# Performance work log

Measured on AMD Instinct MI355X. Metric: run time of the kernel, lower is better.

Reference implementation:

```python
import jax, jax.numpy as jnp
import numpy as np

K = 4096
N = 11008
GROUP_SIZE = 128
NUM_GROUPS = K // GROUP_SIZE
BATCH = 4
SEQ = 2048


def setup_inputs() -> dict:
    key = jax.random.key(0)
    kx, kw, ks = jax.random.split(key, 3)
    x = jax.random.normal(kx, (BATCH, SEQ, K), dtype=jnp.float16)
    # packed uint8 bytes, each holding two INT4 values (stored as int32)
    weight_packed = jax.random.randint(kw, (N, K // 2), 0, 256, dtype=jnp.int32)
    # positive group-wise scales ~ abs(randn)*0.1 -> uniform*0.1 is fine statistically
    scales = (jax.random.uniform(ks, (N, NUM_GROUPS), dtype=jnp.float32) * 0.1).astype(jnp.float16)
    return {"x": x, "weight_packed": weight_packed, "scales": scales}


def _dequantize(weight_packed, scales):
    # unpack: low nibble first, then high nibble -> (N, K) values in [0, 15]
    low = weight_packed & 15
    high = (weight_packed >> 4) & 15
    w_int = jnp.stack([low, high], axis=-1).reshape(weight_packed.shape[0], -1)  # (N, K)
    # symmetric dequant with implicit zero-point 8, group-wise scales
    scales_expanded = jnp.repeat(scales, GROUP_SIZE, axis=1)  # (N, K)
    return scales_expanded * (w_int.astype(jnp.float16) - jnp.float16(8.0))


def reference(x, weight_packed, scales):
    # Y = X @ W_dequant.T : (B, S, K) x (N, K) -> (B, S, N)
    w_dequant = _dequantize(weight_packed, scales)  # (N, K) fp16
    out = jnp.einsum('bsk,nk->bsn', x, w_dequant)
    return out.astype(jnp.float16)
```

## Files before the change

### kernel.cpp

```cpp
#include <hip/hip_runtime.h>
#include <stdint.h>


namespace {

typedef unsigned int u32;
typedef unsigned short u16;
typedef __attribute__((ext_vector_type(8))) short bf16x8;
typedef __attribute__((ext_vector_type(4))) float f32x4;
typedef __attribute__((ext_vector_type(4))) u32 u32x4;

constexpr int Mt = 8192;
constexpr int Nt = 11008;
constexpr int Kt = 4096;
constexpr int KP = Kt / 2;
constexpr int NG = 32;
constexpr int BM = 256;
constexpr int BN = 256;
constexpr int BK = 64;
constexpr int THREADS = 512;
constexpr int GRID = (Mt / BM) * (Nt / BN);
constexpr int NKT = Kt / BK;
constexpr int NB_CNT = Nt / BN;
constexpr int TILE_BYTES = BM * BK * 2;

__device__ __forceinline__ u16 f2bf(float f) {
  u32 u = __float_as_uint(f);
  return (u16)((u + 0x7FFFu + ((u >> 16) & 1u)) >> 16);
}
__device__ __forceinline__ u32 pk2bf(float a, float b) {
  return (u32)f2bf(a) | ((u32)f2bf(b) << 16);
}
__device__ __forceinline__ u32 dqpair(u32 b, float s, float c) {
  float f0 = (float)(b & 15u);
  float f1 = (float)((b >> 4) & 15u);
  return pk2bf(fmaf(f0, s, c), fmaf(f1, s, c));
}
__device__ __forceinline__ void async16(const void* g, void* l) {
  __builtin_amdgcn_global_load_lds(
      (const __attribute__((address_space(1))) u32*)g,
      (__attribute__((address_space(3))) u32*)l, 16, 0, 0);
}

__global__ __launch_bounds__(256) void cvt_x(const float* __restrict__ X,
                                             u32* __restrict__ O) {
  const int total = Mt * Kt / 4;
  for (int j = blockIdx.x * 256 + threadIdx.x; j < total;
       j += (int)(gridDim.x * 256)) {
    float4 v = ((const float4*)X)[j];
    ((uint2*)O)[j] = make_uint2(pk2bf(v.x, v.y), pk2bf(v.z, v.w));
  }
}

__global__ __launch_bounds__(256) void cvt_w(const int* __restrict__ W,
                                             const float* __restrict__ S,
                                             u32* __restrict__ O) {
  const int total = Nt * KP / 4;
  for (int j = blockIdx.x * 256 + threadIdx.x; j < total;
       j += (int)(gridDim.x * 256)) {
    int4 v = ((const int4*)W)[j];
    int vv[4] = {v.x, v.y, v.z, v.w};
    const int j0 = j * 4;
    const int row = j0 >> 11;
    const int jj = j0 & 2047;
    const float* sr = S + (size_t)row * NG;
    u32x4 o;
    #pragma unroll
    for (int e = 0; e < 4; ++e) {
      float s = sr[(jj + e) >> 6];
      o[e] = dqpair((u32)vv[e], s, -8.f * s);
    }
    ((u32x4*)O)[j] = o;
  }
}

__global__ __launch_bounds__(THREADS, 2) void gemm_pre(
    const u16* __restrict__ Xb, const u16* __restrict__ Wb,
    float* __restrict__ Y) {
  __shared__ __align__(16) unsigned char smem[4 * TILE_BYTES];

  const int tid  = (int)threadIdx.x;
  const int lane = tid & 63;
  const int wid  = tid >> 6;
  const int wm   = wid >> 2;
  const int wn   = wid & 3;

  const int bid = (int)blockIdx.x;
  const int wg  = (bid & 7) * (GRID / 8) + (bid >> 3);
  const int mb  = wg / NB_CNT;
  const int nb  = wg - mb * NB_CNT;
  const int m0  = mb * BM;
  const int n0  = nb * BN;

  const int lrow = lane >> 3;
  const int psl  = (lane & 7) ^ lrow;
  const u16* aG = Xb + (size_t)(m0 + wid * 32 + lrow) * Kt + psl * 8;
  const u16* bG = Wb + (size_t)(n0 + wid * 32 + lrow) * Kt + psl * 8;
  const int ldsW = wid * 4096;

  const int frow = lane & 15;
  const int fk   = lane >> 4;
  const int fswz = (lane & 7) << 4;
  const int aRdOff = (wm * 128 + frow) * 128;
  const int bRdOff = (wn * 64 + frow) * 128;

  f32x4 acc[8][4];
  #pragma unroll
  for (int i = 0; i < 8; ++i)
    #pragma unroll
    for (int j = 0; j < 4; ++j) acc[i][j] = f32x4{0.f, 0.f, 0.f, 0.f};

  #define STAGE(b, kt)                                                        \
    do {                                                                      \
      unsigned char* aL = smem + (b) * 2 * TILE_BYTES + ldsW;                 \
      unsigned char* bL = aL + TILE_BYTES;                                    \
      const int koff_ = (kt) * BK;                                            \
      _Pragma("unroll")                                                       \
      for (int i_ = 0; i_ < 4; ++i_) {                                        \
        async16(aG + (size_t)i_ * 8 * Kt + koff_, aL + i_ * 1024);            \
        async16(bG + (size_t)i_ * 8 * Kt + koff_, bL + i_ * 1024);            \
      }                                                                       \
    } while (0)

  STAGE(0, 0);

  #pragma unroll 1
  for (int kt = 0; kt < NKT; ++kt) {
    const int cur = kt & 1;
    if (kt + 1 < NKT) {
      STAGE(cur ^ 1, kt + 1);
      asm volatile("s_waitcnt vmcnt(8)" ::: "memory");
    } else {
      asm volatile("s_waitcnt vmcnt(0)" ::: "memory");
    }
    asm volatile("s_barrier" ::: "memory");

    const unsigned char* aRd = smem + cur * 2 * TILE_BYTES + aRdOff;
    const unsigned char* bRd = aRd + TILE_BYTES - aRdOff + bRdOff;

    #pragma unroll
    for (int kk = 0; kk < 2; ++kk) {
      const int koff = (kk * 64 + fk * 16) ^ fswz;
      bf16x8 af[8], bfr[4];
      #pragma unroll
      for (int fm = 0; fm < 8; ++fm)
        af[fm] = *(const bf16x8*)(aRd + fm * 16 * 128 + koff);
      #pragma unroll
      for (int fn = 0; fn < 4; ++fn)
        bfr[fn] = *(const bf16x8*)(bRd + fn * 16 * 128 + koff);
      __builtin_amdgcn_s_setprio(1);
      #pragma unroll
      for (int fm = 0; fm < 8; ++fm)
        #pragma unroll
        for (int fn = 0; fn < 4; ++fn)
          acc[fm][fn] = __builtin_amdgcn_mfma_f32_16x16x32_bf16(
              af[fm], bfr[fn], acc[fm][fn], 0, 0, 0);
      __builtin_amdgcn_s_setprio(0);
    }

    asm volatile("s_barrier" ::: "memory");
  }
  #undef STAGE

  #pragma unroll
  for (int fm = 0; fm < 8; ++fm) {
    #pragma unroll
    for (int r = 0; r < 4; ++r) {
      const size_t mrow = (size_t)(m0 + wm * 128 + fm * 16 + fk * 4 + r) * Nt;
      #pragma unroll
      for (int fn = 0; fn < 4; ++fn) {
        Y[mrow + (size_t)(n0 + wn * 64 + fn * 16 + frow)] = acc[fm][fn][r];
      }
    }
  }
}

__global__ __launch_bounds__(THREADS) void gemm_fused(
    const float* __restrict__ Xf, const int* __restrict__ W,
    const float* __restrict__ S, float* __restrict__ Y) {
  constexpr int FBN = 128;
  constexpr int FGRID_NB = Nt / FBN;
  __shared__ __align__(16) unsigned char Alds[BM * BK * 2];
  __shared__ __align__(16) unsigned char Blds[FBN * BK * 2];

  const int tid = (int)threadIdx.x;
  const int lane = tid & 63;
  const int wid = tid >> 6;
  const int wm = wid >> 1;
  const int wn = wid & 1;

  const int bid = (int)blockIdx.x;
  const int fgrid = (Mt / BM) * FGRID_NB;
  const int wg = (bid & 7) * (fgrid / 8) + (bid >> 3);
  const int mb = wg / FGRID_NB;
  const int nb = wg - mb * FGRID_NB;
  const int m0 = mb * BM;
  const int n0 = nb * FBN;

  const int frow = lane & 15;
  const int fk = lane >> 4;
  const int fswz = (lane & 7) << 4;
  const unsigned char* aRd = Alds + (wm * 64 + frow) * 128;
  const unsigned char* bRd = Blds + (wn * 64 + frow) * 128;

  f32x4 acc[4][4];
  #pragma unroll
  for (int i = 0; i < 4; ++i)
    #pragma unroll
    for (int j = 0; j < 4; ++j) acc[i][j] = f32x4{0.f, 0.f, 0.f, 0.f};

  const int arow = tid >> 3, acol = tid & 7;
  const float* fA = Xf + (size_t)(m0 + arow) * Kt + acol * 8;
  unsigned char* fAD = Alds + arow * 128 + ((acol ^ (arow & 7)) << 4);
  const int nloc = tid >> 3, c4 = tid & 7;
  const int* fB0 = W + (size_t)(n0 + nloc) * KP + c4 * 4;
  const int* fB1 = fB0 + (size_t)64 * KP;
  const float* sp0 = S + (size_t)(n0 + nloc) * NG;
  const float* sp1 = sp0 + (size_t)64 * NG;
  unsigned char* fBD0 = Blds + nloc * 128 + ((c4 ^ (nloc & 7)) << 4);
  unsigned char* fBD1 = fBD0 + 64 * 128;

  #pragma unroll 1
  for (int kt = 0; kt < NKT; ++kt) {
    const int k0 = kt * BK;
    #pragma unroll
    for (int p = 0; p < 4; ++p) {
      float4 x0 = *(const float4*)(fA + (size_t)p * 64 * Kt + k0);
      float4 x1 = *(const float4*)(fA + (size_t)p * 64 * Kt + k0 + 4);
      u32x4 q;
      q[0] = pk2bf(x0.x, x0.y); q[1] = pk2bf(x0.z, x0.w);
      q[2] = pk2bf(x1.x, x1.y); q[3] = pk2bf(x1.z, x1.w);
      *(u32x4*)(fAD + p * 64 * 128) = q;
    }
    const int g = k0 >> 7;
    const float s0 = sp0[g], s1 = sp1[g];
    const float c0 = -8.f * s0, c1 = -8.f * s1;
    const int4 w0 = *(const int4*)(fB0 + (k0 >> 1));
    const int4 w1 = *(const int4*)(fB1 + (k0 >> 1));
    u32x4 q0, q1;
    q0[0] = dqpair((u32)w0.x, s0, c0); q0[1] = dqpair((u32)w0.y, s0, c0);
    q0[2] = dqpair((u32)w0.z, s0, c0); q0[3] = dqpair((u32)w0.w, s0, c0);
    q1[0] = dqpair((u32)w1.x, s1, c1); q1[1] = dqpair((u32)w1.y, s1, c1);
    q1[2] = dqpair((u32)w1.z, s1, c1); q1[3] = dqpair((u32)w1.w, s1, c1);
    *(u32x4*)fBD0 = q0;
    *(u32x4*)fBD1 = q1;

    __syncthreads();

    #pragma unroll
    for (int kk = 0; kk < 2; ++kk) {
      const int koff = (kk * 64 + fk * 16) ^ fswz;
      bf16x8 af[4], bfr[4];
      #pragma unroll
      for (int fm = 0; fm < 4; ++fm)
        af[fm] = *(const bf16x8*)(aRd + fm * 16 * 128 + koff);
      #pragma unroll
      for (int fn = 0; fn < 4; ++fn)
        bfr[fn] = *(const bf16x8*)(bRd + fn * 16 * 128 + koff);
      #pragma unroll
      for (int fm = 0; fm < 4; ++fm)
        #pragma unroll
        for (int fn = 0; fn < 4; ++fn)
          acc[fm][fn] = __builtin_amdgcn_mfma_f32_16x16x32_bf16(
              af[fm], bfr[fn], acc[fm][fn], 0, 0, 0);
    }
    __syncthreads();
  }

  #pragma unroll
  for (int fm = 0; fm < 4; ++fm) {
    #pragma unroll
    for (int r = 0; r < 4; ++r) {
      const size_t mrow = (size_t)(m0 + wm * 64 + fm * 16 + fk * 4 + r) * Nt;
      #pragma unroll
      for (int fn = 0; fn < 4; ++fn)
        Y[mrow + (size_t)(n0 + wn * 64 + fn * 16 + frow)] = acc[fm][fn][r];
    }
  }
}

}

extern "C" void kernel_launch(void* const* d_in, const int* in_sizes, int n_in,
                              void* d_out, int out_size, void* d_ws, size_t ws_size,
                              hipStream_t stream) {
  (void)in_sizes; (void)n_in; (void)out_size;
  const float* X = (const float*)d_in[0];
  const int* W   = (const int*)d_in[1];
  const float* S = (const float*)d_in[2];
  float* Y       = (float*)d_out;

  const size_t xbytes = (size_t)Mt * Kt * 2;
  const size_t wbytes = (size_t)Nt * Kt * 2;

  if (ws_size >= xbytes + wbytes) {
    u16* Xb = (u16*)d_ws;
    u16* Wb = (u16*)((char*)d_ws + xbytes);
    cvt_x<<<dim3(2048), dim3(256), 0, stream>>>(X, (u32*)Xb);
    cvt_w<<<dim3(2048), dim3(256), 0, stream>>>(W, S, (u32*)Wb);
    gemm_pre<<<dim3(GRID), dim3(THREADS), 0, stream>>>(Xb, Wb, Y);
  } else {
    gemm_fused<<<dim3((Mt / BM) * (Nt / 128)), dim3(THREADS), 0, stream>>>(X, W, S, Y);
  }
}
```

Measured before the change: 805.1 us.

## Restructure bf16 GEMM into 8-phase pipelined schedule with split sub-tile staging

The main GEMM kernel's double-buffered single-stage loop becomes a schedule where each K-tile is split into two A halves and two B halves. Global-to-LDS async loads for upcoming tiles are interleaved between the four MFMA sub-blocks, each gated by vmcnt waits and barriers. LDS use grows to 128KB, and the swizzle and warp mapping change (wm covers 64 rows per sub-block). The aim is to overlap memory traffic with MFMA work more finely and keep LDS reads short. In exchange there are more barriers and a hand-written prologue and epilogue whose vmcnt counts must be exactly right.

Measured after the change: 706.2 us. -12.3%, faster.

```diff
diff --git a/kernel.cpp b/kernel.cpp
--- a/kernel.cpp
+++ b/kernel.cpp
@@ -22,7 +22,6 @@
 constexpr int GRID = (Mt / BM) * (Nt / BN);
 constexpr int NKT = Kt / BK;
 constexpr int NB_CNT = Nt / BN;
-constexpr int TILE_BYTES = BM * BK * 2;
 
 __device__ __forceinline__ u16 f2bf(float f) {
   u32 u = __float_as_uint(f);
@@ -74,10 +73,10 @@
   }
 }
 
-__global__ __launch_bounds__(THREADS, 2) void gemm_pre(
+__global__ __launch_bounds__(THREADS, 2) void gemm8p(
     const u16* __restrict__ Xb, const u16* __restrict__ Wb,
     float* __restrict__ Y) {
-  __shared__ __align__(16) unsigned char smem[4 * TILE_BYTES];
+  __shared__ __align__(16) unsigned char smem[131072];
 
   const int tid  = (int)threadIdx.x;
   const int lane = tid & 63;
@@ -92,17 +91,18 @@
   const int m0  = mb * BM;
   const int n0  = nb * BN;
 
-  const int lrow = lane >> 3;
-  const int psl  = (lane & 7) ^ lrow;
-  const u16* aG = Xb + (size_t)(m0 + wid * 32 + lrow) * Kt + psl * 8;
-  const u16* bG = Wb + (size_t)(n0 + wid * 32 + lrow) * Kt + psl * 8;
-  const int ldsW = wid * 4096;
+  const int srow = tid >> 3;
+  const int sswz = (tid & 7) ^ (srow & 7);
+  const u16* aRow = Xb + (size_t)(m0 + srow) * Kt + sswz * 8;
+  const u16* bRow = Wb + (size_t)(n0 + (srow >> 5) * 64 + (srow & 31)) * Kt + sswz * 8;
+  const int ldst = tid * 16;
 
   const int frow = lane & 15;
   const int fk   = lane >> 4;
-  const int fswz = (lane & 7) << 4;
-  const int aRdOff = (wm * 128 + frow) * 128;
-  const int bRdOff = (wn * 64 + frow) * 128;
+  const int s0o  = ((fk ^ (lane & 7)) << 4);
+  const int s1o  = (((4 + fk) ^ (lane & 7)) << 4);
+  const int aRdC = (wm * 64 + frow) * 128;
+  const int bRdC = (wn * 32 + frow) * 128;
 
   f32x4 acc[8][4];
   #pragma unroll
@@ -110,57 +110,127 @@
     #pragma unroll
     for (int j = 0; j < 4; ++j) acc[i][j] = f32x4{0.f, 0.f, 0.f, 0.f};
 
-  #define STAGE(b, kt)                                                        \
-    do {                                                                      \
-      unsigned char* aL = smem + (b) * 2 * TILE_BYTES + ldsW;                 \
-      unsigned char* bL = aL + TILE_BYTES;                                    \
-      const int koff_ = (kt) * BK;                                            \
-      _Pragma("unroll")                                                       \
-      for (int i_ = 0; i_ < 4; ++i_) {                                        \
-        async16(aG + (size_t)i_ * 8 * Kt + koff_, aL + i_ * 1024);            \
-        async16(bG + (size_t)i_ * 8 * Kt + koff_, bL + i_ * 1024);            \
-      }                                                                       \
-    } while (0)
-
-  STAGE(0, 0);
+  #define GATE(n) asm volatile("s_waitcnt vmcnt(" #n ")" ::: "memory")
+  #define BAR()   asm volatile("s_barrier" ::: "memory")
+
+  #define STAGE_A(g, buf, kt)                                                  \
+    do {                                                                       \
+      unsigned char* d_ = smem + (buf) * 32768 + (g) * 16384 + ldst;           \
+      const u16* s_ = aRow + (size_t)((g) * 64) * Kt + (kt) * 64;              \
+      async16(s_, d_);                                                         \
+      async16(s_ + (size_t)128 * Kt, d_ + 8192);                               \
+    } while (0)
+  #define STAGE_B(p, buf, kt)                                                  \
+    do {                                                                       \
+      unsigned char* d_ = smem + 65536 + (buf) * 32768 + (p) * 16384 + ldst;   \
+      const u16* s_ = bRow + (size_t)((p) * 32) * Kt + (kt) * 64;              \
+      async16(s_, d_);                                                         \
+      async16(s_ + (size_t)128 * Kt, d_ + 8192);                               \
+    } while (0)
+
+  #define LD_A(dst, g, buf)                                                    \
+    do {                                                                       \
+      const unsigned char* b_ = smem + (buf) * 32768 + (g) * 16384 + aRdC;     \
+      _Pragma("unroll")                                                        \
+      for (int q_ = 0; q_ < 4; ++q_) {                                         \
+        dst[q_][0] = *(const bf16x8*)(b_ + q_ * 2048 + s0o);                   \
+        dst[q_][1] = *(const bf16x8*)(b_ + q_ * 2048 + s1o);                   \
+      }                                                                        \
+    } while (0)
+  #define LD_B(dst, p, buf)                                                    \
+    do {                                                                       \
+      const unsigned char* b_ =                                                \
+          smem + 65536 + (buf) * 32768 + (p) * 16384 + bRdC;                   \
+      _Pragma("unroll")                                                        \
+      for (int q_ = 0; q_ < 2; ++q_) {                                         \
+        dst[q_][0] = *(const bf16x8*)(b_ + q_ * 2048 + s0o);                   \
+        dst[q_][1] = *(const bf16x8*)(b_ + q_ * 2048 + s1o);                   \
+      }                                                                        \
+    } while (0)
+
+  #define MM(FG, FNP, A_, B_)                                                  \
+    do {                                                                       \
+      __builtin_amdgcn_s_setprio(1);                                           \
+      _Pragma("unroll")                                                        \
+      for (int fm_ = 0; fm_ < 4; ++fm_)                                        \
+        _Pragma("unroll")                                                      \
+        for (int fn_ = 0; fn_ < 2; ++fn_)                                      \
+          _Pragma("unroll")                                                    \
+          for (int kk_ = 0; kk_ < 2; ++kk_)                                    \
+            acc[(FG) * 4 + fm_][(FNP) * 2 + fn_] =                             \
+                __builtin_amdgcn_mfma_f32_16x16x32_bf16(                       \
+                    A_[fm_][kk_], B_[fn_][kk_],                                \
+                    acc[(FG) * 4 + fm_][(FNP) * 2 + fn_], 0, 0, 0);            \
+      __builtin_amdgcn_s_setprio(0);                                           \
+    } while (0)
+
+  bf16x8 af[4][2], b0[2][2], b1[2][2];
+
+  STAGE_A(0, 0, 0);
+  STAGE_B(0, 0, 0);
+  STAGE_A(1, 0, 0);
+  STAGE_B(1, 0, 0);
+  STAGE_A(0, 1, 1);
+  STAGE_B(0, 1, 1);
+  STAGE_A(1, 1, 1);
 
   #pragma unroll 1
-  for (int kt = 0; kt < NKT; ++kt) {
-    const int cur = kt & 1;
-    if (kt + 1 < NKT) {
-      STAGE(cur ^ 1, kt + 1);
-      asm volatile("s_waitcnt vmcnt(8)" ::: "memory");
-    } else {
-      asm volatile("s_waitcnt vmcnt(0)" ::: "memory");
-    }
-    asm volatile("s_barrier" ::: "memory");
-
-    const unsigned char* aRd = smem + cur * 2 * TILE_BYTES + aRdOff;
-    const unsigned char* bRd = aRd + TILE_BYTES - aRdOff + bRdOff;
-
-    #pragma unroll
-    for (int kk = 0; kk < 2; ++kk) {
-      const int koff = (kk * 64 + fk * 16) ^ fswz;
-      bf16x8 af[8], bfr[4];
-      #pragma unroll
-      for (int fm = 0; fm < 8; ++fm)
-        af[fm] = *(const bf16x8*)(aRd + fm * 16 * 128 + koff);
-      #pragma unroll
-      for (int fn = 0; fn < 4; ++fn)
-        bfr[fn] = *(const bf16x8*)(bRd + fn * 16 * 128 + koff);
-      __builtin_amdgcn_s_setprio(1);
-      #pragma unroll
-      for (int fm = 0; fm < 8; ++fm)
-        #pragma unroll
-        for (int fn = 0; fn < 4; ++fn)
-          acc[fm][fn] = __builtin_amdgcn_mfma_f32_16x16x32_bf16(
-              af[fm], bfr[fn], acc[fm][fn], 0, 0, 0);
-      __builtin_amdgcn_s_setprio(0);
-    }
-
-    asm volatile("s_barrier" ::: "memory");
-  }
-  #undef STAGE
+  for (int t = 0; t < NKT - 2; ++t) {
+    const int b = t & 1;
+    GATE(10); BAR();
+    LD_A(af, 0, b);
+    LD_B(b0, 0, b);
+    STAGE_B(1, b ^ 1, t + 1);
+    MM(0, 0, af, b0);
+    GATE(8); BAR();
+    LD_B(b1, 1, b);
+    STAGE_A(0, b, t + 2);
+    MM(0, 1, af, b1);
+    GATE(12); BAR();
+    LD_A(af, 1, b);
+    STAGE_B(0, b, t + 2);
+    MM(1, 0, af, b0);
+    BAR();
+    STAGE_A(1, b, t + 2);
+    MM(1, 1, af, b1);
+  }
+
+  {
+    GATE(10); BAR();
+    LD_A(af, 0, 0);
+    LD_B(b0, 0, 0);
+    STAGE_B(1, 1, 63);
+    MM(0, 0, af, b0);
+    GATE(8); BAR();
+    LD_B(b1, 1, 0);
+    MM(0, 1, af, b1);
+    GATE(10); BAR();
+    LD_A(af, 1, 0);
+    MM(1, 0, af, b0);
+    BAR();
+    MM(1, 1, af, b1);
+  }
+  {
+    GATE(4); BAR();
+    LD_A(af, 0, 1);
+    LD_B(b0, 0, 1);
+    MM(0, 0, af, b0);
+    GATE(0); BAR();
+    LD_B(b1, 1, 1);
+    MM(0, 1, af, b1);
+    BAR();
+    LD_A(af, 1, 1);
+    MM(1, 0, af, b0);
+    MM(1, 1, af, b1);
+  }
+
+  #undef GATE
+  #undef BAR
+  #undef STAGE_A
+  #undef STAGE_B
+  #undef LD_A
+  #undef LD_B
+  #undef MM
 
   #pragma unroll
   for (int fm = 0; fm < 8; ++fm) {
@@ -175,13 +245,15 @@
   }
 }
 
-__global__ __launch_bounds__(THREADS) void gemm_fused(
+__global__ __launch_bounds__(512) void gemm_fused(
     const float* __restrict__ Xf, const int* __restrict__ W,
     const float* __restrict__ S, float* __restrict__ Y) {
   constexpr int FBN = 128;
-  constexpr int FGRID_NB = Nt / FBN;
-  __shared__ __align__(16) unsigned char Alds[BM * BK * 2];
-  __shared__ __align__(16) unsigned char Blds[FBN * BK * 2];
+  constexpr int FNB = Nt / FBN;
+  constexpr int FBK = 64;
+  constexpr int FNKT = Kt / FBK;
+  __shared__ __align__(16) unsigned char Alds[BM * FBK * 2];
+  __shared__ __align__(16) unsigned char Blds[FBN * FBK * 2];
 
   const int tid = (int)threadIdx.x;
   const int lane = tid & 63;
@@ -190,10 +262,10 @@
   const int wn = wid & 1;
 
   const int bid = (int)blockIdx.x;
-  const int fgrid = (Mt / BM) * FGRID_NB;
+  const int fgrid = (Mt / BM) * FNB;
   const int wg = (bid & 7) * (fgrid / 8) + (bid >> 3);
-  const int mb = wg / FGRID_NB;
-  const int nb = wg - mb * FGRID_NB;
+  const int mb = wg / FNB;
+  const int nb = wg - mb * FNB;
   const int m0 = mb * BM;
   const int n0 = nb * FBN;
 
@@ -221,8 +293,8 @@
   unsigned char* fBD1 = fBD0 + 64 * 128;
 
   #pragma unroll 1
-  for (int kt = 0; kt < NKT; ++kt) {
-    const int k0 = kt * BK;
+  for (int kt = 0; kt < FNKT; ++kt) {
+    const int k0 = kt * FBK;
     #pragma unroll
     for (int p = 0; p < 4; ++p) {
       float4 x0 = *(const float4*)(fA + (size_t)p * 64 * Kt + k0);
@@ -298,8 +370,8 @@
     u16* Wb = (u16*)((char*)d_ws + xbytes);
     cvt_x<<<dim3(2048), dim3(256), 0, stream>>>(X, (u32*)Xb);
     cvt_w<<<dim3(2048), dim3(256), 0, stream>>>(W, S, (u32*)Wb);
-    gemm_pre<<<dim3(GRID), dim3(THREADS), 0, stream>>>(Xb, Wb, Y);
+    gemm8p<<<dim3(GRID), dim3(THREADS), 0, stream>>>(Xb, Wb, Y);
   } else {
-    gemm_fused<<<dim3((Mt / BM) * (Nt / 128)), dim3(THREADS), 0, stream>>>(X, W, S, Y);
-  }
-}
+    gemm_fused<<<dim3((Mt / BM) * (Nt / 128)), dim3(512), 0, stream>>>(X, W, S, Y);
+  }
+}
```
